# Kernel tuning notes

Measured on AMD Instinct MI355X. Metric: run time of the kernel, lower is better.

The kernel has to match this reference:

```python
import jax, jax.numpy as jnp
import numpy as np

B, N = 32, 4096
EMBED_DIM = 256
D = H = W = 64


def setup_inputs() -> dict:
    key = jax.random.key(0)
    k1, k2, k3, k4 = jax.random.split(key, 4)
    points = jax.random.uniform(k1, (B, N, 3), dtype=jnp.float32) * D  # coords in [0, image_size)
    labels = jax.random.randint(k2, (B, N), 0, 2, dtype=jnp.int32)
    pos_embed = jax.random.normal(k3, (1, EMBED_DIM, D, H, W), dtype=jnp.float32) * 0.02
    point_emb = jax.random.normal(k4, (2, EMBED_DIM), dtype=jnp.float32)
    return {"points": points, "labels": labels, "pos_embed": pos_embed, "point_emb": point_emb}


def reference(points, labels, pos_embed, point_emb):
    # int() truncation (coords are non-negative) then clamp to grid bounds
    idx = jnp.clip(points.astype(jnp.int32), 0, jnp.array([D - 1, H - 1, W - 1], dtype=jnp.int32))
    zi, yi, xi = idx[..., 0], idx[..., 1], idx[..., 2]  # each [B, N]
    grid = jnp.transpose(pos_embed[0], (1, 2, 3, 0))  # [D, H, W, C]
    pos_enc = grid[zi, yi, xi]                        # [B, N, C] vectorized gather
    type_emb = point_emb[labels]                      # [B, N, C]
    return pos_enc + type_emb
```

## Files before the change

kernel.cpp:

```cpp
#include <hip/hip_runtime.h>


constexpr int B_ = 32;
constexpr int N_ = 4096;
constexpr int C_ = 256;
constexpr int GD = 64;
constexpr int PTS = B_ * N_;
constexpr int CELLS = GD * GD * GD;
constexpr int NBINS = GD * GD * (GD / 16);
constexpr int CAP = 64;
constexpr int BPB = 8;
constexpr int NBLK = NBINS / BPB;
constexpr int TP = 260;

typedef float f32x4 __attribute__((ext_vector_type(4)));

__device__ __forceinline__ int clamp63(float v) {
    int i = (int)v;
    return min(max(i, 0), GD - 1);
}

__global__ __launch_bounds__(256) void k_scatter(const float* __restrict__ points,
                                                 const int* __restrict__ labels,
                                                 unsigned* __restrict__ counts,
                                                 unsigned* __restrict__ recs,
                                                 const float* __restrict__ pos,
                                                 const float* __restrict__ pemb,
                                                 float* __restrict__ out) {
    int p = blockIdx.x * blockDim.x + threadIdx.x;
    if (p >= PTS) return;
    int zi = clamp63(points[p * 3 + 0]);
    int yi = clamp63(points[p * 3 + 1]);
    int xi = clamp63(points[p * 3 + 2]);
    int key = (zi << 8) | (yi << 2) | (xi >> 4);
    int lab = labels[p];
    unsigned slot = atomicAdd(&counts[key], 1u);
    if (slot < CAP) {
        recs[key * CAP + slot] =
            (unsigned)p | ((unsigned)lab << 17) | ((unsigned)(xi & 15) << 18);
    } else {
        const int cell = (zi << 12) | (yi << 6) | xi;
        for (int c = 0; c < C_; ++c)
            out[(size_t)p * C_ + c] = pos[(size_t)c * CELLS + cell] + pemb[lab * C_ + c];
    }
}

__global__ __launch_bounds__(256) void k_gather(const unsigned* __restrict__ counts,
                                                const unsigned* __restrict__ recs,
                                                const float* __restrict__ pos,
                                                const float* __restrict__ pemb,
                                                float* __restrict__ out) {
    __shared__ float tile[2][16 * TP];

    const int b    = blockIdx.x;
    const int swz  = (b & 7) * (NBLK >> 3) + (b >> 3);
    const int bin0 = swz * BPB;

    const int tid  = threadIdx.x;
    const int w    = tid >> 6;
    const int l    = tid & 63;
    const int o4   = (tid & 3) << 2;
    const int csub = tid >> 2;

    const float4 te0 = *reinterpret_cast<const float4*>(pemb + 4 * l);
    const float4 te1 = *reinterpret_cast<const float4*>(pemb + C_ + 4 * l);

    auto linebase = [](int bin) -> size_t {
        return ((size_t)(bin >> 8) << 12) | ((size_t)((bin >> 2) & 63) << 6) |
               ((size_t)(bin & 3) << 4);
    };

    float4 rv0, rv1, rv2, rv3;
    {
        const size_t lb = linebase(bin0);
        rv0 = *reinterpret_cast<const float4*>(pos + (size_t)(  0 + csub) * CELLS + lb + o4);
        rv1 = *reinterpret_cast<const float4*>(pos + (size_t)( 64 + csub) * CELLS + lb + o4);
        rv2 = *reinterpret_cast<const float4*>(pos + (size_t)(128 + csub) * CELLS + lb + o4);
        rv3 = *reinterpret_cast<const float4*>(pos + (size_t)(192 + csub) * CELLS + lb + o4);
        float* t0 = tile[0];
        t0[(o4 + 0) * TP +   0 + csub] = rv0.x; t0[(o4 + 1) * TP +   0 + csub] = rv0.y;
        t0[(o4 + 2) * TP +   0 + csub] = rv0.z; t0[(o4 + 3) * TP +   0 + csub] = rv0.w;
        t0[(o4 + 0) * TP +  64 + csub] = rv1.x; t0[(o4 + 1) * TP +  64 + csub] = rv1.y;
        t0[(o4 + 2) * TP +  64 + csub] = rv1.z; t0[(o4 + 3) * TP +  64 + csub] = rv1.w;
        t0[(o4 + 0) * TP + 128 + csub] = rv2.x; t0[(o4 + 1) * TP + 128 + csub] = rv2.y;
        t0[(o4 + 2) * TP + 128 + csub] = rv2.z; t0[(o4 + 3) * TP + 128 + csub] = rv2.w;
        t0[(o4 + 0) * TP + 192 + csub] = rv3.x; t0[(o4 + 1) * TP + 192 + csub] = rv3.y;
        t0[(o4 + 2) * TP + 192 + csub] = rv3.z; t0[(o4 + 3) * TP + 192 + csub] = rv3.w;
    }

    for (int k = 0; k < BPB; ++k) {
        const int cur = k & 1;
        if (k + 1 < BPB) {
            const size_t lb = linebase(bin0 + k + 1);
            rv0 = *reinterpret_cast<const float4*>(pos + (size_t)(  0 + csub) * CELLS + lb + o4);
            rv1 = *reinterpret_cast<const float4*>(pos + (size_t)( 64 + csub) * CELLS + lb + o4);
            rv2 = *reinterpret_cast<const float4*>(pos + (size_t)(128 + csub) * CELLS + lb + o4);
            rv3 = *reinterpret_cast<const float4*>(pos + (size_t)(192 + csub) * CELLS + lb + o4);
        }
        __syncthreads();

        const int bin = bin0 + k;
        const unsigned cnt   = min(counts[bin], (unsigned)CAP);
        const unsigned start = (unsigned)bin * CAP;
        const unsigned end   = start + cnt;
        const float* tcur = tile[cur];
        for (unsigned i = start + w; i < end; i += 4) {
            const unsigned rec = recs[i];
            const unsigned p   = rec & 0x1FFFFu;
            const unsigned o   = rec >> 18;
            const float4 te = ((rec >> 17) & 1u) ? te1 : te0;
            const float4 v  = *reinterpret_cast<const float4*>(tcur + o * TP + 4 * l);
            f32x4 rr;
            rr.x = v.x + te.x; rr.y = v.y + te.y; rr.z = v.z + te.z; rr.w = v.w + te.w;
            __builtin_nontemporal_store(rr,
                reinterpret_cast<f32x4*>(out + (size_t)p * C_ + 4 * l));
        }

        if (k + 1 < BPB) {
            float* tn = tile[cur ^ 1];
            tn[(o4 + 0) * TP +   0 + csub] = rv0.x; tn[(o4 + 1) * TP +   0 + csub] = rv0.y;
            tn[(o4 + 2) * TP +   0 + csub] = rv0.z; tn[(o4 + 3) * TP +   0 + csub] = rv0.w;
            tn[(o4 + 0) * TP +  64 + csub] = rv1.x; tn[(o4 + 1) * TP +  64 + csub] = rv1.y;
            tn[(o4 + 2) * TP +  64 + csub] = rv1.z; tn[(o4 + 3) * TP +  64 + csub] = rv1.w;
            tn[(o4 + 0) * TP + 128 + csub] = rv2.x; tn[(o4 + 1) * TP + 128 + csub] = rv2.y;
            tn[(o4 + 2) * TP + 128 + csub] = rv2.z; tn[(o4 + 3) * TP + 128 + csub] = rv2.w;
            tn[(o4 + 0) * TP + 192 + csub] = rv3.x; tn[(o4 + 1) * TP + 192 + csub] = rv3.y;
            tn[(o4 + 2) * TP + 192 + csub] = rv3.z; tn[(o4 + 3) * TP + 192 + csub] = rv3.w;
        }
    }
}

__global__ __launch_bounds__(256) void k_naive(const float* __restrict__ points,
                                               const int* __restrict__ labels,
                                               const float* __restrict__ pos,
                                               const float* __restrict__ pemb,
                                               float* __restrict__ out) {
    const int t    = blockIdx.x * blockDim.x + threadIdx.x;
    const int p    = t >> 6;
    const int lane = t & 63;
    const int c4   = lane << 2;
    if (p >= PTS) return;
    int zi = clamp63(points[p * 3 + 0]);
    int yi = clamp63(points[p * 3 + 1]);
    int xi = clamp63(points[p * 3 + 2]);
    const int cell = (zi << 12) | (yi << 6) | xi;
    const int lab  = labels[p];
    const float4 te = *reinterpret_cast<const float4*>(pemb + lab * C_ + c4);
    const float* g = pos + cell;
    float4 r;
    r.x = g[(c4 + 0) * CELLS] + te.x;
    r.y = g[(c4 + 1) * CELLS] + te.y;
    r.z = g[(c4 + 2) * CELLS] + te.z;
    r.w = g[(c4 + 3) * CELLS] + te.w;
    *reinterpret_cast<float4*>(out + p * C_ + c4) = r;
}

extern "C" void kernel_launch(void* const* d_in, const int* in_sizes, int n_in,
                              void* d_out, int out_size, void* d_ws, size_t ws_size,
                              hipStream_t stream) {
    const float* points = (const float*)d_in[0];
    const int*   labels = (const int*)d_in[1];
    const float* pos    = (const float*)d_in[2];
    const float* pemb   = (const float*)d_in[3];
    float*       out    = (float*)d_out;

    const size_t need = (size_t)(NBINS + NBINS * CAP) * sizeof(unsigned);
    if (ws_size < need) {
        const int total = PTS * 64;
        k_naive<<<(total + 255) / 256, 256, 0, stream>>>(points, labels, pos, pemb, out);
        return;
    }
    unsigned* counts = (unsigned*)d_ws;
    unsigned* recs   = counts + NBINS;

    hipMemsetAsync(counts, 0, NBINS * sizeof(unsigned), stream);
    k_scatter<<<(PTS + 255) / 256, 256, 0, stream>>>(points, labels, counts, recs,
                                                     pos, pemb, out);
    k_gather<<<NBLK, 256, 0, stream>>>(counts, recs, pos, pemb, out);
}
```

Measured before the change: 97.91 us.

## Stage grid tiles via direct global-to-LDS loads with XOR swizzle

Replaces the register-staged, transposed shared-memory fill with direct global_load_lds copies into a channel-major tile, using an XOR swizzle on the x offset to spread bank accesses. The gather phase now reads four scalar LDS values per output instead of one float4 from a padded transposed tile. The goal is to cut register pressure and VALU/LDS-store work in staging and to overlap the async copy with the write-out phase. The risks are more LDS read instructions per output and relying on async-load completion ordering at the barrier without an explicit vmcnt wait.

Result: no change. 99.39 us (+1.5%).

```diff
diff --git a/kernel.cpp b/kernel.cpp
--- a/kernel.cpp
+++ b/kernel.cpp
@@ -11,13 +11,17 @@
 constexpr int CAP = 64;
 constexpr int BPB = 8;
 constexpr int NBLK = NBINS / BPB;
-constexpr int TP = 260;
 
 typedef float f32x4 __attribute__((ext_vector_type(4)));
 
 __device__ __forceinline__ int clamp63(float v) {
     int i = (int)v;
     return min(max(i, 0), GD - 1);
+}
+
+__device__ __forceinline__ size_t linebase(int bin) {
+    return ((size_t)(bin >> 8) << 12) | ((size_t)((bin >> 2) & 63) << 6) |
+           ((size_t)(bin & 3) << 4);
 }
 
 __global__ __launch_bounds__(256) void k_scatter(const float* __restrict__ points,
@@ -50,83 +54,65 @@
                                                 const float* __restrict__ pos,
                                                 const float* __restrict__ pemb,
                                                 float* __restrict__ out) {
-    __shared__ float tile[2][16 * TP];
+    __shared__ float tile[2][C_ * 16];
 
     const int b    = blockIdx.x;
     const int swz  = (b & 7) * (NBLK >> 3) + (b >> 3);
     const int bin0 = swz * BPB;
 
-    const int tid  = threadIdx.x;
-    const int w    = tid >> 6;
-    const int l    = tid & 63;
-    const int o4   = (tid & 3) << 2;
-    const int csub = tid >> 2;
+    const int tid = threadIdx.x;
+    const int w   = tid >> 6;
+    const int l   = tid & 63;
 
     const float4 te0 = *reinterpret_cast<const float4*>(pemb + 4 * l);
     const float4 te1 = *reinterpret_cast<const float4*>(pemb + C_ + 4 * l);
 
-    auto linebase = [](int bin) -> size_t {
-        return ((size_t)(bin >> 8) << 12) | ((size_t)((bin >> 2) & 63) << 6) |
-               ((size_t)(bin & 3) << 4);
+    const int lsub = l >> 2;
+    const int gq   = (((l & 3) ^ ((l >> 4) & 3)) << 2);
+
+    auto stage = [&](float* lbuf, int bin) {
+        const size_t lb = linebase(bin);
+        #pragma unroll
+        for (int i = 0; i < 4; ++i) {
+            const int chunk = (w << 6) + (i << 4);
+            const float* src = pos + (size_t)(chunk + lsub) * CELLS + lb + gq;
+            float* dst = lbuf + chunk * 16;
+            __builtin_amdgcn_global_load_lds(
+                (const __attribute__((address_space(1))) unsigned int*)src,
+                (__attribute__((address_space(3))) unsigned int*)dst,
+                16, 0, 0);
+        }
     };
 
-    float4 rv0, rv1, rv2, rv3;
-    {
-        const size_t lb = linebase(bin0);
-        rv0 = *reinterpret_cast<const float4*>(pos + (size_t)(  0 + csub) * CELLS + lb + o4);
-        rv1 = *reinterpret_cast<const float4*>(pos + (size_t)( 64 + csub) * CELLS + lb + o4);
-        rv2 = *reinterpret_cast<const float4*>(pos + (size_t)(128 + csub) * CELLS + lb + o4);
-        rv3 = *reinterpret_cast<const float4*>(pos + (size_t)(192 + csub) * CELLS + lb + o4);
-        float* t0 = tile[0];
-        t0[(o4 + 0) * TP +   0 + csub] = rv0.x; t0[(o4 + 1) * TP +   0 + csub] = rv0.y;
-        t0[(o4 + 2) * TP +   0 + csub] = rv0.z; t0[(o4 + 3) * TP +   0 + csub] = rv0.w;
-        t0[(o4 + 0) * TP +  64 + csub] = rv1.x; t0[(o4 + 1) * TP +  64 + csub] = rv1.y;
-        t0[(o4 + 2) * TP +  64 + csub] = rv1.z; t0[(o4 + 3) * TP +  64 + csub] = rv1.w;
-        t0[(o4 + 0) * TP + 128 + csub] = rv2.x; t0[(o4 + 1) * TP + 128 + csub] = rv2.y;
-        t0[(o4 + 2) * TP + 128 + csub] = rv2.z; t0[(o4 + 3) * TP + 128 + csub] = rv2.w;
-        t0[(o4 + 0) * TP + 192 + csub] = rv3.x; t0[(o4 + 1) * TP + 192 + csub] = rv3.y;
-        t0[(o4 + 2) * TP + 192 + csub] = rv3.z; t0[(o4 + 3) * TP + 192 + csub] = rv3.w;
-    }
-
-    for (int k = 0; k < BPB; ++k) {
-        const int cur = k & 1;
-        if (k + 1 < BPB) {
-            const size_t lb = linebase(bin0 + k + 1);
-            rv0 = *reinterpret_cast<const float4*>(pos + (size_t)(  0 + csub) * CELLS + lb + o4);
-            rv1 = *reinterpret_cast<const float4*>(pos + (size_t)( 64 + csub) * CELLS + lb + o4);
-            rv2 = *reinterpret_cast<const float4*>(pos + (size_t)(128 + csub) * CELLS + lb + o4);
-            rv3 = *reinterpret_cast<const float4*>(pos + (size_t)(192 + csub) * CELLS + lb + o4);
-        }
-        __syncthreads();
-
-        const int bin = bin0 + k;
+    auto phase2 = [&](int bin, const float* tcur) {
         const unsigned cnt   = min(counts[bin], (unsigned)CAP);
         const unsigned start = (unsigned)bin * CAP;
         const unsigned end   = start + cnt;
-        const float* tcur = tile[cur];
         for (unsigned i = start + w; i < end; i += 4) {
             const unsigned rec = recs[i];
             const unsigned p   = rec & 0x1FFFFu;
             const unsigned o   = rec >> 18;
             const float4 te = ((rec >> 17) & 1u) ? te1 : te0;
-            const float4 v  = *reinterpret_cast<const float4*>(tcur + o * TP + 4 * l);
+            const int xi = ((((int)o >> 2) ^ (l & 3)) << 2) | ((int)o & 3);
             f32x4 rr;
-            rr.x = v.x + te.x; rr.y = v.y + te.y; rr.z = v.z + te.z; rr.w = v.w + te.w;
+            rr.x = tcur[(4 * l + 0) * 16 + xi] + te.x;
+            rr.y = tcur[(4 * l + 1) * 16 + xi] + te.y;
+            rr.z = tcur[(4 * l + 2) * 16 + xi] + te.z;
+            rr.w = tcur[(4 * l + 3) * 16 + xi] + te.w;
             __builtin_nontemporal_store(rr,
                 reinterpret_cast<f32x4*>(out + (size_t)p * C_ + 4 * l));
         }
+    };
 
-        if (k + 1 < BPB) {
-            float* tn = tile[cur ^ 1];
-            tn[(o4 + 0) * TP +   0 + csub] = rv0.x; tn[(o4 + 1) * TP +   0 + csub] = rv0.y;
-            tn[(o4 + 2) * TP +   0 + csub] = rv0.z; tn[(o4 + 3) * TP +   0 + csub] = rv0.w;
-            tn[(o4 + 0) * TP +  64 + csub] = rv1.x; tn[(o4 + 1) * TP +  64 + csub] = rv1.y;
-            tn[(o4 + 2) * TP +  64 + csub] = rv1.z; tn[(o4 + 3) * TP +  64 + csub] = rv1.w;
-            tn[(o4 + 0) * TP + 128 + csub] = rv2.x; tn[(o4 + 1) * TP + 128 + csub] = rv2.y;
-            tn[(o4 + 2) * TP + 128 + csub] = rv2.z; tn[(o4 + 3) * TP + 128 + csub] = rv2.w;
-            tn[(o4 + 0) * TP + 192 + csub] = rv3.x; tn[(o4 + 1) * TP + 192 + csub] = rv3.y;
-            tn[(o4 + 2) * TP + 192 + csub] = rv3.z; tn[(o4 + 3) * TP + 192 + csub] = rv3.w;
-        }
+    stage(tile[0], bin0);
+    __syncthreads();
+
+    #pragma unroll
+    for (int k = 0; k < BPB; ++k) {
+        const int cur = k & 1;
+        if (k + 1 < BPB) stage(tile[cur ^ 1], bin0 + k + 1);
+        phase2(bin0 + k, tile[cur]);
+        __syncthreads();
     }
 }
 
```
